# Kernel tuning notes

Measured on AMD Instinct MI355X. Metric: run time of the kernel, lower is better.

## Reference

```python
import jax, jax.numpy as jnp
import numpy as np

WIN = 25  # win_size (odd) -> AvgPool1d preserves time length
PAD = (WIN - 1) // 2

def _avg_pool_same(xc):
    xp = jnp.pad(xc, ((0, 0), (0, 0), (PAD, PAD)))
    cs = jnp.cumsum(xp, axis=-1)
    zero = jnp.zeros(cs.shape[:-1] + (1,), cs.dtype)
    cs = jnp.concatenate([zero, cs], axis=-1)
    win_sum = cs[..., WIN:] - cs[..., :-WIN]  # [b, c, time]
    return win_sum / WIN

def setup_inputs() -> dict:
    key = jax.random.key(0)
    ks = jax.random.split(key, 5)
    B, S, C, P = 64, 720, 321, 336
    scale = 1.0 / np.sqrt(S)  # mimic nn.Linear init scale
    return {
        "x": jax.random.normal(ks[0], (B, S, C), jnp.float32),
        "W_res": jax.random.uniform(ks[1], (C, P, S), jnp.float32, -scale, scale),
        "b_res": jax.random.uniform(ks[2], (C, P), jnp.float32, -scale, scale),
        "W_trend": jax.random.uniform(ks[3], (C, P, S), jnp.float32, -scale, scale),
        "b_trend": jax.random.uniform(ks[4], (C, P), jnp.float32, -scale, scale),
    }

def reference(x, W_res, b_res, W_trend, b_trend):
    # x: [batch, seq_len, channel] -> [batch, channel, seq_len]
    xc = jnp.transpose(x, (0, 2, 1))
    season = _avg_pool_same(xc)            # trend (called 'mean' in torch code)
    res = xc - season
    # Per-channel Linear loop fused as one batched matmul over channels.
    res_out = jnp.einsum('bcs,cps->bcp', res, W_res) + b_res[None]
    trend_out = jnp.einsum('bcs,cps->bcp', season, W_trend) + b_trend[None]
    return res_out + trend_out  # [batch, channel, pred_len]
```

## Files before the change

kernel.cpp:

```cpp
#include <hip/hip_runtime.h>
#include <hip/hip_bf16.h>

#define B_ 64
#define S_ 720
#define C_ 321
#define P_ 336
#define SP 736
#define WIN 25
#define PADW 12
#define NTILE 112
#define KSTEPS 23
#define CT 8
#define AQ_PER_MAT 1890048

typedef __bf16 bf16x8 __attribute__((ext_vector_type(8)));
typedef float f32x4 __attribute__((ext_vector_type(4)));

__device__ __forceinline__ unsigned short f2bf(float f) {
  unsigned int u = __builtin_bit_cast(unsigned int, f);
  u += 0x7FFFu + ((u >> 16) & 1u);
  return (unsigned short)(u >> 16);
}

__global__ __launch_bounds__(256) void pass0_decomp(
    const float* __restrict__ x,
    uint4* __restrict__ resQ,
    uint4* __restrict__ seaQ) {
  __shared__ float xs[CT][745];
  __shared__ unsigned short obuf[2 * CT * SP];
  int c0 = blockIdx.x * CT;
  int b = blockIdx.y;
  int t = threadIdx.x;

  if (t < CT * 24) {
    int c = t / 24, h = t % 24;
    xs[c][h < 12 ? h : h + 720] = 0.f;
  }
  {
    int m = t >> 7, c = (t >> 4) & 7, s = 720 + (t & 15);
    obuf[(m * CT + c) * SP + s] = 0;
  }
  {
    int c = t & 7;
    int svalid = (c0 + c < C_);
    for (int p = 0; p < 23; ++p) {
      int s = (t >> 3) + p * 32;
      if (s < S_ && svalid) xs[c][PADW + s] = x[(b * S_ + s) * C_ + c0 + c];
    }
  }
  __syncthreads();
  {
    int c = t & 7;
    int s0 = (t >> 3) * 23;
    int s1 = s0 + 23; if (s1 > S_) s1 = S_;
    float wsum = 0.f;
#pragma unroll
    for (int j = 0; j < WIN; ++j) wsum += xs[c][s0 + j];
    for (int s = s0; s < s1; ++s) {
      float sea = wsum * (1.0f / WIN);
      float res = xs[c][s + PADW] - sea;
      obuf[c * SP + s] = f2bf(res);
      obuf[(CT + c) * SP + s] = f2bf(sea);
      wsum += xs[c][s + WIN] - xs[c][s];
    }
  }
  __syncthreads();
  const uint4* ob = (const uint4*)obuf;
  for (int i = t; i < 2 * CT * 92; i += 256) {
    int row = i / 92;
    int off = i - row * 92;
    int c = row & 7;
    int m = row >> 3;
    if (c0 + c < C_) {
      uint4* dst = m ? seaQ : resQ;
      dst[((c0 + c) * B_ + b) * 92 + off] = ob[row * 92 + off];
    }
  }
}

__global__ __launch_bounds__(256) void gemm_fused(
    const uint4* __restrict__ abase,
    const float4* __restrict__ wR,
    const float4* __restrict__ wT,
    const float* __restrict__ bR,
    const float* __restrict__ bT,
    float* __restrict__ out) {
  __shared__ __align__(16) unsigned char lds[10240 + 17920 + 448];
  unsigned char* ldsA = lds;
  unsigned char* ldsB = lds + 10240;
  float* bsum = (float*)(lds + 10240 + 17920);

  int blk = blockIdx.x;
  int c = blk / 3;
  int nt = blk - c * 3;
  int p0 = nt * NTILE;
  int t = threadIdx.x;
  int w = t >> 6;
  int lane = t & 63;
  int col = lane & 15;
  int quad = lane >> 4;

  if (t < NTILE) bsum[t] = bR[c * P_ + p0 + t] + bT[c * P_ + p0 + t];

  int aOffG[2], aOffL[2];
#pragma unroll
  for (int i = 0; i < 2; ++i) {
    int idx = i * 256 + t;
    int m = idx >> 8;
    int r = (idx >> 2) & 63;
    int k16 = idx & 3;
    aOffG[i] = m * AQ_PER_MAT + c * 5888 + r * 92 + k16;
    aOffL[i] = m * 5120 + r * 80 + k16 * 16;
  }
  int bOffG[7], bOffL[7], bK4[7], bM[7];
#pragma unroll
  for (int i = 0; i < 7; ++i) {
    int idx = i * 256 + t;
    int m = idx / 896;
    int rem = idx - m * 896;
    int r = rem >> 3;
    int k4 = rem & 7;
    bM[i] = m;
    bK4[i] = k4;
    bOffG[i] = c * 60480 + (p0 + r) * 180 + k4;
    bOffL[i] = m * 8960 + r * 80 + k4 * 8;
  }

  f32x4 acc[7];
#pragma unroll
  for (int i = 0; i < 7; ++i) acc[i] = (f32x4){0.f, 0.f, 0.f, 0.f};

  int aFragOff = (w * 16 + col) * 80 + quad * 16;

  uint4 av[2];
  float4 bv[7];
#pragma unroll
  for (int i = 0; i < 2; ++i) av[i] = abase[aOffG[i]];
#pragma unroll
  for (int i = 0; i < 7; ++i) {
    float4 v = {0.f, 0.f, 0.f, 0.f};
    if (bK4[i] * 4 < S_) {
      const float4* src = bM[i] ? wT : wR;
      v = src[bOffG[i]];
    }
    bv[i] = v;
  }

  for (int ks = 0; ks < KSTEPS; ++ks) {
    __syncthreads();
#pragma unroll
    for (int i = 0; i < 2; ++i) *(uint4*)(ldsA + aOffL[i]) = av[i];
#pragma unroll
    for (int i = 0; i < 7; ++i) {
      ushort4 pk;
      pk.x = f2bf(bv[i].x); pk.y = f2bf(bv[i].y);
      pk.z = f2bf(bv[i].z); pk.w = f2bf(bv[i].w);
      *(ushort4*)(ldsB + bOffL[i]) = pk;
    }
    __syncthreads();
    if (ks + 1 < KSTEPS) {
      int kn = ks + 1;
#pragma unroll
      for (int i = 0; i < 2; ++i) av[i] = abase[aOffG[i] + kn * 4];
#pragma unroll
      for (int i = 0; i < 7; ++i) {
        float4 v = {0.f, 0.f, 0.f, 0.f};
        if (kn * 32 + bK4[i] * 4 < S_) {
          const float4* src = bM[i] ? wT : wR;
          v = src[bOffG[i] + kn * 8];
        }
        bv[i] = v;
      }
    }
    bf16x8 aR = *(const bf16x8*)(ldsA + aFragOff);
    bf16x8 aS = *(const bf16x8*)(ldsA + 5120 + aFragOff);
#pragma unroll
    for (int tt = 0; tt < 7; ++tt) {
      int bo = (tt * 16 + col) * 80 + quad * 16;
      bf16x8 bRf = *(const bf16x8*)(ldsB + bo);
      bf16x8 bTf = *(const bf16x8*)(ldsB + 8960 + bo);
      acc[tt] = __builtin_amdgcn_mfma_f32_16x16x32_bf16(aR, bRf, acc[tt], 0, 0, 0);
      acc[tt] = __builtin_amdgcn_mfma_f32_16x16x32_bf16(aS, bTf, acc[tt], 0, 0, 0);
    }
  }

#pragma unroll
  for (int r = 0; r < 4; ++r) {
    int brow = w * 16 + quad * 4 + r;
#pragma unroll
    for (int tt = 0; tt < 7; ++tt) {
      int p = p0 + tt * 16 + col;
      out[(brow * C_ + c) * P_ + p] = acc[tt][r] + bsum[tt * 16 + col];
    }
  }
}

extern "C" void kernel_launch(void* const* d_in, const int* in_sizes, int n_in,
                              void* d_out, int out_size, void* d_ws, size_t ws_size,
                              hipStream_t stream) {
  const float* x = (const float*)d_in[0];
  const float4* wR = (const float4*)d_in[1];
  const float* bR = (const float*)d_in[2];
  const float4* wT = (const float4*)d_in[3];
  const float* bT = (const float*)d_in[4];
  float* out = (float*)d_out;

  uint4* resQ = (uint4*)d_ws;
  uint4* seaQ = resQ + AQ_PER_MAT;

  dim3 g0((C_ + CT - 1) / CT, B_);
  pass0_decomp<<<g0, 256, 0, stream>>>(x, resQ, seaQ);
  gemm_fused<<<C_ * 3, 256, 0, stream>>>((const uint4*)d_ws, wR, wT, bR, bT, out);
}
```

Measured before the change: 746.6 us.

## Double-buffer global prefetch two k-steps ahead with explicit waitcnt and barriers

Moves the GEMM main loop to two register buffer sets, so the global loads for step k+2 are issued while step k is staged and computed. Hand-placed vmcnt/lgkmcnt waits, raw s_barrier and sched_barrier calls keep memory latency overlapped with the MFMA work. Out-of-range weight loads now clamp the address instead of branching, and the bias sum is read from global in the epilogue rather than staged through LDS. The cost is more register pressure from the doubled buffers, and the hand-written wait counts are fragile.

```diff
diff --git a/kernel.cpp b/kernel.cpp
--- a/kernel.cpp
+++ b/kernel.cpp
@@ -9,6 +9,7 @@
 #define WIN 25
 #define PADW 12
 #define NTILE 112
+#define NTPC 3
 #define KSTEPS 23
 #define CT 8
 #define AQ_PER_MAT 1890048
@@ -85,22 +86,19 @@
     const float* __restrict__ bR,
     const float* __restrict__ bT,
     float* __restrict__ out) {
-  __shared__ __align__(16) unsigned char lds[10240 + 17920 + 448];
+  __shared__ __align__(16) unsigned char lds[10240 + 17920];
   unsigned char* ldsA = lds;
   unsigned char* ldsB = lds + 10240;
-  float* bsum = (float*)(lds + 10240 + 17920);
 
   int blk = blockIdx.x;
-  int c = blk / 3;
-  int nt = blk - c * 3;
+  int c = blk / NTPC;
+  int nt = blk - c * NTPC;
   int p0 = nt * NTILE;
   int t = threadIdx.x;
   int w = t >> 6;
   int lane = t & 63;
   int col = lane & 15;
   int quad = lane >> 4;
-
-  if (t < NTILE) bsum[t] = bR[c * P_ + p0 + t] + bT[c * P_ + p0 + t];
 
   int aOffG[2], aOffL[2];
 #pragma unroll
@@ -112,7 +110,7 @@
     aOffG[i] = m * AQ_PER_MAT + c * 5888 + r * 92 + k16;
     aOffL[i] = m * 5120 + r * 80 + k16 * 16;
   }
-  int bOffG[7], bOffL[7], bK4[7], bM[7];
+  int bOffG[7], bOffL[7], bLim[7], bM[7];
 #pragma unroll
   for (int i = 0; i < 7; ++i) {
     int idx = i * 256 + t;
@@ -121,7 +119,7 @@
     int r = rem >> 3;
     int k4 = rem & 7;
     bM[i] = m;
-    bK4[i] = k4;
+    bLim[i] = S_ - k4 * 4;
     bOffG[i] = c * 60480 + (p0 + r) * 180 + k4;
     bOffL[i] = m * 8960 + r * 80 + k4 * 8;
   }
@@ -132,65 +130,83 @@
 
   int aFragOff = (w * 16 + col) * 80 + quad * 16;
 
-  uint4 av[2];
-  float4 bv[7];
-#pragma unroll
-  for (int i = 0; i < 2; ++i) av[i] = abase[aOffG[i]];
-#pragma unroll
-  for (int i = 0; i < 7; ++i) {
-    float4 v = {0.f, 0.f, 0.f, 0.f};
-    if (bK4[i] * 4 < S_) {
-      const float4* src = bM[i] ? wT : wR;
-      v = src[bOffG[i]];
-    }
-    bv[i] = v;
-  }
-
-  for (int ks = 0; ks < KSTEPS; ++ks) {
-    __syncthreads();
-#pragma unroll
-    for (int i = 0; i < 2; ++i) *(uint4*)(ldsA + aOffL[i]) = av[i];
-#pragma unroll
-    for (int i = 0; i < 7; ++i) {
-      ushort4 pk;
-      pk.x = f2bf(bv[i].x); pk.y = f2bf(bv[i].y);
-      pk.z = f2bf(bv[i].z); pk.w = f2bf(bv[i].w);
-      *(ushort4*)(ldsB + bOffL[i]) = pk;
-    }
-    __syncthreads();
-    if (ks + 1 < KSTEPS) {
-      int kn = ks + 1;
-#pragma unroll
-      for (int i = 0; i < 2; ++i) av[i] = abase[aOffG[i] + kn * 4];
-#pragma unroll
-      for (int i = 0; i < 7; ++i) {
-        float4 v = {0.f, 0.f, 0.f, 0.f};
-        if (kn * 32 + bK4[i] * 4 < S_) {
-          const float4* src = bM[i] ? wT : wR;
-          v = src[bOffG[i] + kn * 8];
-        }
-        bv[i] = v;
-      }
-    }
-    bf16x8 aR = *(const bf16x8*)(ldsA + aFragOff);
-    bf16x8 aS = *(const bf16x8*)(ldsA + 5120 + aFragOff);
-#pragma unroll
-    for (int tt = 0; tt < 7; ++tt) {
-      int bo = (tt * 16 + col) * 80 + quad * 16;
-      bf16x8 bRf = *(const bf16x8*)(ldsB + bo);
-      bf16x8 bTf = *(const bf16x8*)(ldsB + 8960 + bo);
-      acc[tt] = __builtin_amdgcn_mfma_f32_16x16x32_bf16(aR, bRf, acc[tt], 0, 0, 0);
-      acc[tt] = __builtin_amdgcn_mfma_f32_16x16x32_bf16(aS, bTf, acc[tt], 0, 0, 0);
-    }
-  }
-
+  uint4 av0[2], av1[2];
+  float4 bv0[7], bv1[7];
+
+#define ISSUE(av, bv, kn)                                                     \
+  {                                                                           \
+    _Pragma("unroll")                                                         \
+    for (int i = 0; i < 2; ++i) av[i] = abase[aOffG[i] + (kn) * 4];           \
+    _Pragma("unroll")                                                         \
+    for (int i = 0; i < 7; ++i) {                                             \
+      const float4* s = bM[i] ? wT : wR;                                      \
+      int off = bOffG[i] + (((kn) * 32 < bLim[i]) ? (kn) * 8 : 0);            \
+      bv[i] = s[off];                                                         \
+    }                                                                         \
+  }
+
+#define STAGE_AND_COMPUTE(av, bv, kn_next, doIssue)                           \
+  {                                                                           \
+    __builtin_amdgcn_s_barrier();                                             \
+    _Pragma("unroll")                                                         \
+    for (int i = 0; i < 2; ++i) *(uint4*)(ldsA + aOffL[i]) = av[i];           \
+    _Pragma("unroll")                                                         \
+    for (int i = 0; i < 7; ++i) {                                             \
+      ushort4 pk;                                                             \
+      pk.x = f2bf(bv[i].x); pk.y = f2bf(bv[i].y);                             \
+      pk.z = f2bf(bv[i].z); pk.w = f2bf(bv[i].w);                             \
+      *(ushort4*)(ldsB + bOffL[i]) = pk;                                      \
+    }                                                                         \
+    if (doIssue) ISSUE(av, bv, kn_next)                                       \
+    asm volatile("s_waitcnt lgkmcnt(0)" ::: "memory");                        \
+    __builtin_amdgcn_sched_barrier(0);                                        \
+    __builtin_amdgcn_s_barrier();                                             \
+    __builtin_amdgcn_sched_barrier(0);                                        \
+    bf16x8 aR = *(const bf16x8*)(ldsA + aFragOff);                            \
+    bf16x8 aS = *(const bf16x8*)(ldsA + 5120 + aFragOff);                     \
+    _Pragma("unroll")                                                         \
+    for (int tt = 0; tt < 7; ++tt) {                                          \
+      int bo = (tt * 16 + col) * 80 + quad * 16;                              \
+      bf16x8 bRf = *(const bf16x8*)(ldsB + bo);                               \
+      bf16x8 bTf = *(const bf16x8*)(ldsB + 8960 + bo);                        \
+      acc[tt] = __builtin_amdgcn_mfma_f32_16x16x32_bf16(aR, bRf, acc[tt], 0, 0, 0); \
+      acc[tt] = __builtin_amdgcn_mfma_f32_16x16x32_bf16(aS, bTf, acc[tt], 0, 0, 0); \
+    }                                                                         \
+  }
+
+  ISSUE(av0, bv0, 0)
+  asm volatile("" ::: "memory");
+  ISSUE(av1, bv1, 1)
+
+#pragma unroll 1
+  for (int ks = 0; ks + 2 < KSTEPS; ks += 2) {
+    asm volatile("s_waitcnt vmcnt(9)" ::: "memory");
+    __builtin_amdgcn_sched_barrier(0);
+    STAGE_AND_COMPUTE(av0, bv0, ks + 2, true)
+    asm volatile("s_waitcnt vmcnt(9)" ::: "memory");
+    __builtin_amdgcn_sched_barrier(0);
+    STAGE_AND_COMPUTE(av1, bv1, ks + 3, (ks + 3 < KSTEPS))
+  }
+  asm volatile("s_waitcnt vmcnt(0)" ::: "memory");
+  __builtin_amdgcn_sched_barrier(0);
+  STAGE_AND_COMPUTE(av0, bv0, 0, false)
+
+#undef ISSUE
+#undef STAGE_AND_COMPUTE
+
+  float bias[7];
+#pragma unroll
+  for (int tt = 0; tt < 7; ++tt) {
+    int p = c * P_ + p0 + tt * 16 + col;
+    bias[tt] = bR[p] + bT[p];
+  }
 #pragma unroll
   for (int r = 0; r < 4; ++r) {
     int brow = w * 16 + quad * 4 + r;
 #pragma unroll
     for (int tt = 0; tt < 7; ++tt) {
       int p = p0 + tt * 16 + col;
-      out[(brow * C_ + c) * P_ + p] = acc[tt][r] + bsum[tt * 16 + col];
+      out[(brow * C_ + c) * P_ + p] = acc[tt][r] + bias[tt];
     }
   }
 }
@@ -210,5 +226,5 @@
 
   dim3 g0((C_ + CT - 1) / CT, B_);
   pass0_decomp<<<g0, 256, 0, stream>>>(x, resQ, seaQ);
-  gemm_fused<<<C_ * 3, 256, 0, stream>>>((const uint4*)d_ws, wR, wT, bR, bT, out);
-}
+  gemm_fused<<<C_ * NTPC, 256, 0, stream>>>((const uint4*)d_ws, wR, wT, bR, bT, out);
+}
```

Measured after the change: 735.3 us. Within noise of the previous version (-1.5%).
